# Kernel tuning notes

Hardware: AMD Instinct MI355X
Metric: run time of the kernel (lower is better)

## Reference

```python
import jax, jax.numpy as jnp
import numpy as np

V, SMAX, D, H, L, DFF, W = 32000, 1024, 1024, 16, 2, 4096, 256
HD = D // H
EPS = 1e-6


def setup_inputs() -> dict:
    key = jax.random.key(0)
    ks = jax.random.split(key, 20)
    s = lambda k, shape, scale=0.02: jax.random.normal(k, shape, dtype=jnp.float32) * scale
    return {
        "input_ids": jax.random.randint(ks[0], (2, SMAX), 0, V, dtype=jnp.int64),
        "emb": s(ks[1], (V, D)),
        "pos": s(ks[2], (SMAX, D)),
        "norm1_w": jnp.ones((L, D), jnp.float32),
        "norm2_w": jnp.ones((L, D), jnp.float32),
        "wq": s(ks[3], (L, D, D)), "bq": jnp.zeros((L, D), jnp.float32),
        "wk": s(ks[4], (L, D, D)), "bk": jnp.zeros((L, D), jnp.float32),
        "wv": s(ks[5], (L, D, D)), "bv": jnp.zeros((L, D), jnp.float32),
        "wo": s(ks[6], (L, D, D)), "bo": jnp.zeros((L, D), jnp.float32),
        "w1": s(ks[7], (L, D, DFF)), "b1": jnp.zeros((L, DFF), jnp.float32),
        "w2": s(ks[8], (L, DFF, D)), "b2": jnp.zeros((L, D), jnp.float32),
        "normf_w": jnp.ones((D,), jnp.float32),
    }


def rms(x, w):
    return x * jax.lax.rsqrt(jnp.mean(x * x, axis=-1, keepdims=True) + EPS) * w


def reference(input_ids, emb, pos, norm1_w, norm2_w, wq, bq, wk, bk, wv, bv,
              wo, bo, w1, b1, w2, b2, normf_w):
    B, S = input_ids.shape
    x = emb[input_ids] + pos[:S]  # [B,S,D]
    # sliding-window causal mask: attend to j with 0 <= i-j < W
    i = jnp.arange(S)[:, None]
    j = jnp.arange(S)[None, :]
    mask = (j <= i) & (i - j < W)  # [S,S]
    neg = jnp.asarray(-1e9, x.dtype)
    for l in range(L):
        h = rms(x, norm1_w[l])
        q = (h @ wq[l] + bq[l]).reshape(B, S, H, HD)
        k = (h @ wk[l] + bk[l]).reshape(B, S, H, HD)
        v = (h @ wv[l] + bv[l]).reshape(B, S, H, HD)
        scores = jnp.einsum('bqhd,bkhd->bhqk', q, k) / np.sqrt(HD).astype(np.float32)
        scores = jnp.where(mask[None, None], scores, neg)
        attn = jax.nn.softmax(scores, axis=-1)
        o = jnp.einsum('bhqk,bkhd->bqhd', attn, v).reshape(B, S, D)
        x = x + (o @ wo[l] + bo[l])
        h2 = rms(x, norm2_w[l])
        x = x + (jax.nn.gelu(h2 @ w1[l] + b1[l], approximate=False) @ w2[l] + b2[l])
    x = rms(x, normf_w)
    logits = x @ emb.T  # tied lm_head
    return logits
```

## Files before the change

kernel.cpp:

```cpp
#include <hip/hip_runtime.h>
#include <hip/hip_bf16.h>
#include <cstdint>

typedef __bf16 bf16;
typedef __bf16 bf16x8 __attribute__((ext_vector_type(8)));
typedef __bf16 bf16x4 __attribute__((ext_vector_type(4)));
typedef float  f32x4  __attribute__((ext_vector_type(4)));

constexpr int V_    = 32000;
constexpr int SMAX_ = 1024;
constexpr int D_    = 1024;
constexpr int H_    = 16;
constexpr int L_    = 2;
constexpr int DFF_  = 4096;
constexpr int WIN_  = 256;
constexpr int B_    = 2;
constexpr int M_    = B_ * SMAX_;

#define SBAR0_() __builtin_amdgcn_sched_barrier(0)
#define HWBAR_() { __builtin_amdgcn_s_barrier(); SBAR0_(); }
#define LGKM0_() { asm volatile("s_waitcnt lgkmcnt(0)" ::: "memory"); SBAR0_(); }

__global__ __launch_bounds__(512) void gemm_lm_bdirect(
    const bf16* __restrict__ A, const bf16* __restrict__ BT,
    float* __restrict__ outf, int Nn)
{
  constexpr int KK = 1024, NT = 16;
  __shared__ __align__(16) bf16 ldsA[2][16384];

  const int t = threadIdx.x, lane = t & 63, w = t >> 6;
  const int l16 = lane & 15, lh = lane >> 4;
  const int wm = w >> 2, wn = w & 3;

  const int nloc = gridDim.x >> 3;
  const int wg = (blockIdx.x & 7) * nloc + (blockIdx.x >> 3);
  const long m0 = (long)(wg & 7) * 256;
  const long n0 = (long)(wg >> 3) * 256;

  auto STGA = [&](int c, int k0) {
    #pragma unroll
    for (int q = 0; q < 4; ++q) {
      int row = q * 64 + (t >> 3);
      int sl  = (t & 7) ^ (row & 7);
      const bf16* g = A + (m0 + row) * (long)KK + k0 + sl * 8;
      __builtin_amdgcn_global_load_lds(
          (const __attribute__((address_space(1))) uint32_t*)g,
          (__attribute__((address_space(3))) uint32_t*)(&ldsA[c][q * 4096 + t * 8]),
          16, 0, 0);
    }
  };
  auto LDA = [&](int c, int mi, int ks) -> bf16x8 {
    int row = wm * 128 + mi * 16 + l16;
    int sl  = (ks * 4 + lh) ^ (row & 7);
    return *(const bf16x8*)(&ldsA[c][row * 64 + sl * 8]);
  };
  auto BADDR = [&](int ni, int kk) -> const bf16* {
    return BT + (n0 + wn * 64 + ni * 16 + l16) * (long)KK + kk + lh * 8;
  };

  f32x4 acc[8][4] = {};
  bf16x8 a[8], b0[4], b1[4];

  STGA(0, 0);
  SBAR0_();
  #pragma unroll
  for (int ni = 0; ni < 4; ++ni) b0[ni] = *(const bf16x8*)BADDR(ni, 0);

  for (int j = 0; j < NT; ++j) {
    const int c = j & 1;
    const int kc = j * 64;
    const int kn = (kc + 64) & (KK - 1);
    asm volatile("s_waitcnt vmcnt(4)" ::: "memory"); SBAR0_();
    HWBAR_();
    #pragma unroll
    for (int mi = 0; mi < 8; ++mi) a[mi] = LDA(c, mi, 0);
    #pragma unroll
    for (int ni = 0; ni < 4; ++ni) b1[ni] = *(const bf16x8*)BADDR(ni, kc + 32);
    LGKM0_();
    asm volatile("s_waitcnt vmcnt(4)" ::: "memory"); SBAR0_();
    __builtin_amdgcn_s_setprio(1);
    #pragma unroll
    for (int mi = 0; mi < 8; ++mi)
      #pragma unroll
      for (int ni = 0; ni < 4; ++ni)
        acc[mi][ni] = __builtin_amdgcn_mfma_f32_16x16x32_bf16(a[mi], b0[ni], acc[mi][ni], 0, 0, 0);
    __builtin_amdgcn_s_setprio(0);
    SBAR0_();
    #pragma unroll
    for (int mi = 0; mi < 8; ++mi) a[mi] = LDA(c, mi, 1);
    STGA(c ^ 1, kn);
    SBAR0_();
    #pragma unroll
    for (int ni = 0; ni < 4; ++ni) b0[ni] = *(const bf16x8*)BADDR(ni, kn);
    LGKM0_();
    asm volatile("s_waitcnt vmcnt(8)" ::: "memory"); SBAR0_();
    __builtin_amdgcn_s_setprio(1);
    #pragma unroll
    for (int mi = 0; mi < 8; ++mi)
      #pragma unroll
      for (int ni = 0; ni < 4; ++ni)
        acc[mi][ni] = __builtin_amdgcn_mfma_f32_16x16x32_bf16(a[mi], b1[ni], acc[mi][ni], 0, 0, 0);
    __builtin_amdgcn_s_setprio(0);
  }

  asm volatile("s_waitcnt vmcnt(0) lgkmcnt(0)" ::: "memory");
  #pragma unroll
  for (int mi = 0; mi < 8; ++mi)
    #pragma unroll
    for (int ni = 0; ni < 4; ++ni)
      #pragma unroll
      for (int rr = 0; rr < 4; ++rr) {
        long row = m0 + wm * 128 + mi * 16 + lh * 4 + rr;
        long col = n0 + wn * 64 + ni * 16 + l16;
        outf[row * Nn + col] = acc[mi][ni][rr];
      }
}

template<int BM, int EPI>
__global__ __launch_bounds__(256, (BM == 128 ? 2 : 3)) void gemm_deep(
    const bf16* __restrict__ A, const bf16* __restrict__ BT,
    const float* __restrict__ bias, float* __restrict__ resid,
    bf16* __restrict__ outb, float* __restrict__ outf,
    int Nn, int Kk, int nbyMask, int nbyShift)
{
  constexpr int WR = BM / 32;
  constexpr int CA = BM / 64;
  constexpr int LPS = CA + 2;
  __shared__ __align__(16) bf16 ldsA[4 * BM * 32];
  __shared__ __align__(16) bf16 ldsB[4 * 4096];

  const int t = threadIdx.x, lane = t & 63, w = t >> 6;
  const int l16 = lane & 15, lh = lane >> 4;
  const int wm = w >> 1, wn = w & 1;

  const int nwg = gridDim.x, bid = blockIdx.x;
  const int nloc = nwg >> 3;
  const int wg = (bid & 7) * nloc + (bid >> 3);
  const long m0 = (long)(wg & nbyMask) * BM;
  const long n0 = (long)(wg >> nbyShift) * 128;

  auto STGA = [&](bf16* dst, int k0) {
    #pragma unroll
    for (int j = 0; j < CA; ++j) {
      int p = j * 4096 + t * 16;
      int row = p >> 6;
      int sl = ((p >> 4) & 3) ^ (row & 3);
      const bf16* g = A + (m0 + row) * (long)Kk + k0 + sl * 8;
      __builtin_amdgcn_global_load_lds(
          (const __attribute__((address_space(1))) uint32_t*)g,
          (__attribute__((address_space(3))) uint32_t*)(dst + j * 2048 + w * 512),
          16, 0, 0);
    }
  };
  auto STGB = [&](bf16* dst, int k0) {
    #pragma unroll
    for (int j = 0; j < 2; ++j) {
      int p = j * 4096 + t * 16;
      int row = p >> 6;
      int sl = ((p >> 4) & 3) ^ (row & 3);
      const bf16* g = BT + (n0 + row) * (long)Kk + k0 + sl * 8;
      __builtin_amdgcn_global_load_lds(
          (const __attribute__((address_space(1))) uint32_t*)g,
          (__attribute__((address_space(3))) uint32_t*)(dst + j * 2048 + w * 512),
          16, 0, 0);
    }
  };
  auto LDF = [&](const bf16* base, int rowb) -> bf16x8 {
    int row = rowb + l16;
    return *(const bf16x8*)(base + row * 32 + ((lh ^ (l16 & 3)) << 3));
  };

  f32x4 acc[WR][4] = {};

  STGA(ldsA,               0);  STGB(ldsB,        0);
  STGA(ldsA + BM * 32,    32);  STGB(ldsB + 4096, 32);
  STGA(ldsA + 2 * BM * 32, 64); STGB(ldsB + 8192, 64);
  int kNext = 96;

  const int NT = Kk >> 5;
  for (int i = 0; i < NT; ++i) {
    const int cur = i & 3, nb = (i + 3) & 3;
    if constexpr (LPS == 4) { asm volatile("s_waitcnt vmcnt(8)" ::: "memory"); }
    else                    { asm volatile("s_waitcnt vmcnt(6)" ::: "memory"); }
    SBAR0_();
    HWBAR_();
    const bf16* Ac = ldsA + cur * BM * 32;
    const bf16* Bc = ldsB + cur * 4096;
    bf16x8 af[WR], bb[4];
    #pragma unroll
    for (int mi = 0; mi < WR; ++mi) af[mi] = LDF(Ac, wm * (WR * 16) + mi * 16);
    #pragma unroll
    for (int ni = 0; ni < 4; ++ni) bb[ni] = LDF(Bc, wn * 64 + ni * 16);
    STGA(ldsA + nb * BM * 32, kNext);
    STGB(ldsB + nb * 4096, kNext);
    kNext += 32; if (kNext == Kk) kNext = 0;
    LGKM0_();
    __builtin_amdgcn_s_setprio(1);
    #pragma unroll
    for (int mi = 0; mi < WR; ++mi)
      #pragma unroll
      for (int ni = 0; ni < 4; ++ni)
        acc[mi][ni] = __builtin_amdgcn_mfma_f32_16x16x32_bf16(af[mi], bb[ni], acc[mi][ni], 0, 0, 0);
    __builtin_amdgcn_s_setprio(0);
  }

  #pragma unroll
  for (int mi = 0; mi < WR; ++mi)
    #pragma unroll
    for (int ni = 0; ni < 4; ++ni)
      #pragma unroll
      for (int rr = 0; rr < 4; ++rr) {
        long row = m0 + wm * (WR * 16) + mi * 16 + lh * 4 + rr;
        long col = n0 + wn * 64 + ni * 16 + l16;
        float v = acc[mi][ni][rr];
        if (EPI == 0) {
          outb[row * Nn + col] = (bf16)(v + bias[col]);
        } else if (EPI == 1) {
          float xx = v + bias[col];
          outb[row * Nn + col] = (bf16)(0.5f * xx * (1.0f + erff(xx * 0.70710678118654752f)));
        } else if (EPI == 2) {
          resid[row * Nn + col] += v + bias[col];
        } else {
          outf[row * Nn + col] = v;
        }
      }
}

__global__ __launch_bounds__(256) void attn_swa(
    const bf16* __restrict__ qkv, bf16* __restrict__ o)
{
  constexpr int PADK = 72;
  constexpr int PADV = 40;
  __shared__ bf16 Qs[64 * PADK];
  __shared__ bf16 Ks[32 * PADK];
  __shared__ bf16 Vt[64 * PADV];
  __shared__ bf16 Ps[4][16 * PADV];

  const int bid = blockIdx.x;
  const int qb = bid & 15;
  const int h  = (bid >> 4) & 15;
  const int b  = bid >> 8;
  const int q0 = qb * 64;
  const int t = threadIdx.x, lane = t & 63, w = t >> 6;
  const int l16 = lane & 15, lh = lane >> 4;

  #pragma unroll
  for (int i = 0; i < 2; i++) {
    int e = t + i * 256;
    int row = e >> 3, cc = e & 7;
    uint4 g = *(const uint4*)(qkv + ((long)(b * SMAX_ + q0 + row)) * 3072 + h * 64 + cc * 8);
    *(uint4*)(Qs + row * PADK + cc * 8) = g;
  }
  __syncthreads();
  bf16x8 aq[2];
  const int qrow = w * 16 + l16;
  #pragma unroll
  for (int ks = 0; ks < 2; ks++)
    aq[ks] = *(const bf16x8*)(Qs + qrow * PADK + ks * 32 + lh * 8);

  float m_run[4], l_run[4];
  f32x4 oacc[4];
  #pragma unroll
  for (int rr = 0; rr < 4; rr++) { m_run[rr] = -1e30f; l_run[rr] = 0.0f; }
  #pragma unroll
  for (int n = 0; n < 4; n++) oacc[n] = (f32x4){0.f, 0.f, 0.f, 0.f};

  const int tlo = q0 - (WIN_ - 1);
  const int jlo = (tlo <= 0) ? 0 : (tlo & ~31);
  const int iq  = q0 + w * 16 + lh * 4;

  for (int j0 = jlo; j0 < q0 + 64; j0 += 32) {
    __syncthreads();
    {
      int row = t >> 3, cc = t & 7;
      long base = ((long)(b * SMAX_ + j0 + row)) * 3072 + h * 64 + cc * 8;
      uint4 gk = *(const uint4*)(qkv + base + 1024);
      *(uint4*)(Ks + row * PADK + cc * 8) = gk;
      bf16x8 vv = *(const bf16x8*)(qkv + base + 2048);
      #pragma unroll
      for (int j = 0; j < 8; j++)
        Vt[(cc * 8 + j) * PADV + row] = vv[j];
    }
    __syncthreads();

    f32x4 s[2] = {(f32x4){0.f,0.f,0.f,0.f}, (f32x4){0.f,0.f,0.f,0.f}};
    #pragma unroll
    for (int nt = 0; nt < 2; nt++)
      #pragma unroll
      for (int ks = 0; ks < 2; ks++) {
        bf16x8 bk = *(const bf16x8*)(Ks + (nt * 16 + l16) * PADK + ks * 32 + lh * 8);
        s[nt] = __builtin_amdgcn_mfma_f32_16x16x32_bf16(aq[ks], bk, s[nt], 0, 0, 0);
      }

    float sc[2][4];
    #pragma unroll
    for (int nt = 0; nt < 2; nt++)
      #pragma unroll
      for (int rr = 0; rr < 4; rr++) {
        int i = iq + rr;
        int j = j0 + nt * 16 + l16;
        float v = s[nt][rr] * 0.125f;
        bool ok = (j <= i) && (i - j < WIN_);
        sc[nt][rr] = ok ? v : -1e30f;
      }

    float pb[2][4], alpha[4];
    #pragma unroll
    for (int rr = 0; rr < 4; rr++) {
      float mt = fmaxf(sc[0][rr], sc[1][rr]);
      #pragma unroll
      for (int off = 1; off < 16; off <<= 1) mt = fmaxf(mt, __shfl_xor(mt, off, 64));
      float mn = fmaxf(m_run[rr], mt);
      float a = __expf(m_run[rr] - mn);
      m_run[rr] = mn; alpha[rr] = a;
      float p0 = __expf(sc[0][rr] - mn);
      float p1 = __expf(sc[1][rr] - mn);
      pb[0][rr] = p0; pb[1][rr] = p1;
      float ls = p0 + p1;
      #pragma unroll
      for (int off = 1; off < 16; off <<= 1) ls += __shfl_xor(ls, off, 64);
      l_run[rr] = l_run[rr] * a + ls;
    }
    #pragma unroll
    for (int n = 0; n < 4; n++)
      #pragma unroll
      for (int rr = 0; rr < 4; rr++) oacc[n][rr] *= alpha[rr];

    #pragma unroll
    for (int rr = 0; rr < 4; rr++) {
      int prow = lh * 4 + rr;
      Ps[w][prow * PADV + l16]      = (bf16)pb[0][rr];
      Ps[w][prow * PADV + 16 + l16] = (bf16)pb[1][rr];
    }
    __syncthreads();

    bf16x8 pa = *(const bf16x8*)(&Ps[w][l16 * PADV + lh * 8]);
    #pragma unroll
    for (int n = 0; n < 4; n++) {
      bf16x8 bv = *(const bf16x8*)(Vt + (n * 16 + l16) * PADV + lh * 8);
      oacc[n] = __builtin_amdgcn_mfma_f32_16x16x32_bf16(pa, bv, oacc[n], 0, 0, 0);
    }
  }

  #pragma unroll
  for (int rr = 0; rr < 4; rr++) {
    int i = iq + rr;
    float inv = 1.0f / l_run[rr];
    #pragma unroll
    for (int n = 0; n < 4; n++)
      o[((long)(b * SMAX_ + i)) * D_ + h * 64 + n * 16 + l16] = (bf16)(oacc[n][rr] * inv);
  }
}

__global__ __launch_bounds__(256) void transpose_cvt(
    const float* __restrict__ src, bf16* __restrict__ dst,
    int Kk, int Nn, long srcL, long dstL)
{
  __shared__ float tile[32][33];
  const int tx = threadIdx.x, ty = threadIdx.y;
  const long n0 = (long)blockIdx.x * 32, k0 = (long)blockIdx.y * 32;
  src += (long)blockIdx.z * srcL;
  dst += (long)blockIdx.z * dstL;
  #pragma unroll
  for (int i = 0; i < 4; i++)
    tile[ty + i * 8][tx] = src[(k0 + ty + i * 8) * Nn + n0 + tx];
  __syncthreads();
  #pragma unroll
  for (int i = 0; i < 4; i++)
    dst[(n0 + ty + i * 8) * Kk + k0 + tx] = (bf16)tile[tx][ty + i * 8];
}

__global__ __launch_bounds__(256) void cvt_bf16(
    const float* __restrict__ src, bf16* __restrict__ dst, long n4)
{
  long i = (long)blockIdx.x * 256 + threadIdx.x;
  if (i >= n4) return;
  float4 v = ((const float4*)src)[i];
  bf16x4 o; o[0] = (bf16)v.x; o[1] = (bf16)v.y; o[2] = (bf16)v.z; o[3] = (bf16)v.w;
  ((bf16x4*)dst)[i] = o;
}

__global__ __launch_bounds__(256) void pack_bqkv(
    const float* __restrict__ bq, const float* __restrict__ bk,
    const float* __restrict__ bv, float* __restrict__ out)
{
  int i = blockIdx.x * 256 + threadIdx.x;
  if (i >= L_ * 3072) return;
  int l = i / 3072, c = i % 3072;
  float v = (c < 1024) ? bq[l * 1024 + c]
          : (c < 2048) ? bk[l * 1024 + c - 1024]
                       : bv[l * 1024 + c - 2048];
  out[i] = v;
}

__global__ __launch_bounds__(256) void embed_k(
    const int* __restrict__ ids, const float* __restrict__ emb,
    const float* __restrict__ pos, float* __restrict__ x)
{
  const int m = blockIdx.x, t = threadIdx.x;
  const int id = ids[m];
  const int s = m & (SMAX_ - 1);
  float4 e = ((const float4*)(emb + (long)id * D_))[t];
  float4 p = ((const float4*)(pos + (long)s * D_))[t];
  float4 rr; rr.x = e.x + p.x; rr.y = e.y + p.y; rr.z = e.z + p.z; rr.w = e.w + p.w;
  ((float4*)(x + (long)m * D_))[t] = rr;
}

__global__ __launch_bounds__(256) void rmsnorm_k(
    const float* __restrict__ x, const float* __restrict__ wgt,
    bf16* __restrict__ out)
{
  __shared__ float red[4];
  const int m = blockIdx.x, t = threadIdx.x;
  float4 v = ((const float4*)(x + (long)m * D_))[t];
  float ss = v.x * v.x + v.y * v.y + v.z * v.z + v.w * v.w;
  #pragma unroll
  for (int off = 1; off < 64; off <<= 1) ss += __shfl_xor(ss, off, 64);
  const int lane = t & 63, w = t >> 6;
  if (lane == 0) red[w] = ss;
  __syncthreads();
  float tot = red[0] + red[1] + red[2] + red[3];
  float rs = rsqrtf(tot * (1.0f / D_) + 1e-6f);
  float4 g = ((const float4*)wgt)[t];
  bf16x4 o;
  o[0] = (bf16)(v.x * rs * g.x); o[1] = (bf16)(v.y * rs * g.y);
  o[2] = (bf16)(v.z * rs * g.z); o[3] = (bf16)(v.w * rs * g.w);
  ((bf16x4*)(out + (long)m * D_))[t] = o;
}

extern "C" void kernel_launch(void* const* d_in, const int* in_sizes, int n_in,
                              void* d_out, int out_size, void* d_ws, size_t ws_size,
                              hipStream_t stream)
{
  const int*   ids = (const int*)d_in[0];
  const float* emb = (const float*)d_in[1];
  const float* pos = (const float*)d_in[2];
  const float* n1w = (const float*)d_in[3];
  const float* n2w = (const float*)d_in[4];
  const float* wq  = (const float*)d_in[5];
  const float* bq  = (const float*)d_in[6];
  const float* wk  = (const float*)d_in[7];
  const float* bk  = (const float*)d_in[8];
  const float* wv  = (const float*)d_in[9];
  const float* bv  = (const float*)d_in[10];
  const float* wo  = (const float*)d_in[11];
  const float* bo  = (const float*)d_in[12];
  const float* w1  = (const float*)d_in[13];
  const float* b1  = (const float*)d_in[14];
  const float* w2  = (const float*)d_in[15];
  const float* b2  = (const float*)d_in[16];
  const float* nfw = (const float*)d_in[17];

  char* p = (char*)d_ws;
  auto alloc = [&](size_t bytes) {
    char* rr = p; p += (bytes + 255) & ~(size_t)255; return rr;
  };
  bf16*  wqkv_t = (bf16*) alloc((size_t)L_ * 3 * 1024 * 1024 * 2);
  bf16*  wo_t   = (bf16*) alloc((size_t)L_ * 1024 * 1024 * 2);
  bf16*  w1_t   = (bf16*) alloc((size_t)L_ * 4096 * 1024 * 2);
  bf16*  w2_t   = (bf16*) alloc((size_t)L_ * 1024 * 4096 * 2);
  bf16*  emb_bf = (bf16*) alloc((size_t)V_ * D_ * 2);
  float* bqkv   = (float*)alloc((size_t)L_ * 3072 * 4);
  float* x      = (float*)alloc((size_t)M_ * D_ * 4);
  bf16*  hbuf   = (bf16*) alloc((size_t)M_ * D_ * 2);
  bf16*  qkv    = (bf16*) alloc((size_t)M_ * 3072 * 2);
  bf16*  obuf   = (bf16*) alloc((size_t)M_ * D_ * 2);
  bf16*  ff     = (bf16*) alloc((size_t)M_ * DFF_ * 2);

  const dim3 b32(32, 8, 1);
  transpose_cvt<<<dim3(32, 32, L_),  b32, 0, stream>>>(wq, wqkv_t,                1024, 1024, 1024 * 1024, 3 * 1024 * 1024);
  transpose_cvt<<<dim3(32, 32, L_),  b32, 0, stream>>>(wk, wqkv_t + 1024 * 1024,  1024, 1024, 1024 * 1024, 3 * 1024 * 1024);
  transpose_cvt<<<dim3(32, 32, L_),  b32, 0, stream>>>(wv, wqkv_t + 2*1024*1024,  1024, 1024, 1024 * 1024, 3 * 1024 * 1024);
  transpose_cvt<<<dim3(32, 32, L_),  b32, 0, stream>>>(wo, wo_t,                  1024, 1024, 1024 * 1024, 1024 * 1024);
  transpose_cvt<<<dim3(128, 32, L_), b32, 0, stream>>>(w1, w1_t,                  1024, 4096, 1024 * 4096, 4096 * 1024);
  transpose_cvt<<<dim3(32, 128, L_), b32, 0, stream>>>(w2, w2_t,                  4096, 1024, 4096 * 1024, 1024 * 4096);
  cvt_bf16<<<32000, 256, 0, stream>>>(emb, emb_bf, (long)V_ * D_ / 4);
  pack_bqkv<<<24, 256, 0, stream>>>(bq, bk, bv, bqkv);
  embed_k<<<M_, 256, 0, stream>>>(ids, emb, pos, x);

  for (int l = 0; l < L_; l++) {
    rmsnorm_k<<<M_, 256, 0, stream>>>(x, n1w + l * D_, hbuf);
    gemm_deep<128, 0><<<dim3(16 * 24), 256, 0, stream>>>(
        hbuf, wqkv_t + (size_t)l * 3 * 1024 * 1024, bqkv + l * 3072,
        nullptr, qkv, nullptr, 3072, 1024, 15, 4);
    attn_swa<<<B_ * H_ * (SMAX_ / 64), 256, 0, stream>>>(qkv, obuf);
    gemm_deep<64, 2><<<dim3(32 * 8), 256, 0, stream>>>(
        obuf, wo_t + (size_t)l * 1024 * 1024, bo + l * D_,
        x, nullptr, nullptr, 1024, 1024, 31, 5);
    rmsnorm_k<<<M_, 256, 0, stream>>>(x, n2w + l * D_, hbuf);
    gemm_deep<128, 1><<<dim3(16 * 32), 256, 0, stream>>>(
        hbuf, w1_t + (size_t)l * 4096 * 1024, b1 + l * DFF_,
        nullptr, ff, nullptr, 4096, 1024, 15, 4);
    gemm_deep<64, 2><<<dim3(32 * 8), 256, 0, stream>>>(
        ff, w2_t + (size_t)l * 1024 * 4096, b2 + l * D_,
        x, nullptr, nullptr, 1024, 4096, 31, 5);
  }
  rmsnorm_k<<<M_, 256, 0, stream>>>(x, nfw, hbuf);
  gemm_lm_bdirect<<<dim3(8 * (V_ / 256)), 512, 0, stream>>>(
      hbuf, emb_bf, (float*)d_out, V_);
}
```

Measured before the change: 650.1 us.

## Restructure LM-head and layer GEMMs with LDS-staged B tiles and new pipelines

Measured after the change: 640.9 us. About the same (-1.4%).

```diff
diff --git a/kernel.cpp b/kernel.cpp
--- a/kernel.cpp
+++ b/kernel.cpp
@@ -21,21 +21,22 @@
 #define HWBAR_() { __builtin_amdgcn_s_barrier(); SBAR0_(); }
 #define LGKM0_() { asm volatile("s_waitcnt lgkmcnt(0)" ::: "memory"); SBAR0_(); }
 
-__global__ __launch_bounds__(512) void gemm_lm_bdirect(
+__global__ __launch_bounds__(512, 1) void gemm_lm2(
     const bf16* __restrict__ A, const bf16* __restrict__ BT,
     float* __restrict__ outf, int Nn)
 {
   constexpr int KK = 1024, NT = 16;
-  __shared__ __align__(16) bf16 ldsA[2][16384];
+  __shared__ __align__(16) bf16 ldsA[3][16384];
+  __shared__ __align__(16) bf16 ldsB[3][8192];
 
   const int t = threadIdx.x, lane = t & 63, w = t >> 6;
   const int l16 = lane & 15, lh = lane >> 4;
-  const int wm = w >> 2, wn = w & 3;
+  const int wm = w >> 1, wn = w & 1;
 
   const int nloc = gridDim.x >> 3;
   const int wg = (blockIdx.x & 7) * nloc + (blockIdx.x >> 3);
   const long m0 = (long)(wg & 7) * 256;
-  const long n0 = (long)(wg >> 3) * 256;
+  const long n0 = (long)(wg >> 3) * 128;
 
   auto STGA = [&](int c, int k0) {
     #pragma unroll
@@ -49,85 +50,95 @@
           16, 0, 0);
     }
   };
+  auto STGB = [&](int c, int k0) {
+    #pragma unroll
+    for (int q = 0; q < 2; ++q) {
+      int row = q * 64 + (t >> 3);
+      int sl  = (t & 7) ^ (row & 7);
+      const bf16* g = BT + (n0 + row) * (long)KK + k0 + sl * 8;
+      __builtin_amdgcn_global_load_lds(
+          (const __attribute__((address_space(1))) uint32_t*)g,
+          (__attribute__((address_space(3))) uint32_t*)(&ldsB[c][q * 4096 + t * 8]),
+          16, 0, 0);
+    }
+  };
   auto LDA = [&](int c, int mi, int ks) -> bf16x8 {
-    int row = wm * 128 + mi * 16 + l16;
+    int row = wm * 64 + mi * 16 + l16;
     int sl  = (ks * 4 + lh) ^ (row & 7);
     return *(const bf16x8*)(&ldsA[c][row * 64 + sl * 8]);
   };
-  auto BADDR = [&](int ni, int kk) -> const bf16* {
-    return BT + (n0 + wn * 64 + ni * 16 + l16) * (long)KK + kk + lh * 8;
-  };
-
-  f32x4 acc[8][4] = {};
-  bf16x8 a[8], b0[4], b1[4];
-
-  STGA(0, 0);
-  SBAR0_();
-  #pragma unroll
-  for (int ni = 0; ni < 4; ++ni) b0[ni] = *(const bf16x8*)BADDR(ni, 0);
+  auto LDB = [&](int c, int ni, int ks) -> bf16x8 {
+    int row = wn * 64 + ni * 16 + l16;
+    int sl  = (ks * 4 + lh) ^ (row & 7);
+    return *(const bf16x8*)(&ldsB[c][row * 64 + sl * 8]);
+  };
+
+  f32x4 acc[4][4] = {};
+  bf16x8 a[4], b[4];
+
+  STGA(0, 0);  STGB(0, 0);
+  STGA(1, 64); STGB(1, 64);
+  int kNext = 128, stg = 2, c = 0;
 
   for (int j = 0; j < NT; ++j) {
-    const int c = j & 1;
-    const int kc = j * 64;
-    const int kn = (kc + 64) & (KK - 1);
-    asm volatile("s_waitcnt vmcnt(4)" ::: "memory"); SBAR0_();
+    asm volatile("s_waitcnt vmcnt(6)" ::: "memory"); SBAR0_();
     HWBAR_();
     #pragma unroll
-    for (int mi = 0; mi < 8; ++mi) a[mi] = LDA(c, mi, 0);
-    #pragma unroll
-    for (int ni = 0; ni < 4; ++ni) b1[ni] = *(const bf16x8*)BADDR(ni, kc + 32);
+    for (int mi = 0; mi < 4; ++mi) a[mi] = LDA(c, mi, 0);
+    #pragma unroll
+    for (int ni = 0; ni < 4; ++ni) b[ni] = LDB(c, ni, 0);
+    STGA(stg, kNext);
     LGKM0_();
-    asm volatile("s_waitcnt vmcnt(4)" ::: "memory"); SBAR0_();
     __builtin_amdgcn_s_setprio(1);
     #pragma unroll
-    for (int mi = 0; mi < 8; ++mi)
+    for (int mi = 0; mi < 4; ++mi)
       #pragma unroll
       for (int ni = 0; ni < 4; ++ni)
-        acc[mi][ni] = __builtin_amdgcn_mfma_f32_16x16x32_bf16(a[mi], b0[ni], acc[mi][ni], 0, 0, 0);
+        acc[mi][ni] = __builtin_amdgcn_mfma_f32_16x16x32_bf16(a[mi], b[ni], acc[mi][ni], 0, 0, 0);
     __builtin_amdgcn_s_setprio(0);
-    SBAR0_();
-    #pragma unroll
-    for (int mi = 0; mi < 8; ++mi) a[mi] = LDA(c, mi, 1);
-    STGA(c ^ 1, kn);
-    SBAR0_();
-    #pragma unroll
-    for (int ni = 0; ni < 4; ++ni) b0[ni] = *(const bf16x8*)BADDR(ni, kn);
+    HWBAR_();
+    #pragma unroll
+    for (int mi = 0; mi < 4; ++mi) a[mi] = LDA(c, mi, 1);
+    #pragma unroll
+    for (int ni = 0; ni < 4; ++ni) b[ni] = LDB(c, ni, 1);
+    STGB(stg, kNext);
     LGKM0_();
-    asm volatile("s_waitcnt vmcnt(8)" ::: "memory"); SBAR0_();
     __builtin_amdgcn_s_setprio(1);
     #pragma unroll
-    for (int mi = 0; mi < 8; ++mi)
+    for (int mi = 0; mi < 4; ++mi)
       #pragma unroll
       for (int ni = 0; ni < 4; ++ni)
-        acc[mi][ni] = __builtin_amdgcn_mfma_f32_16x16x32_bf16(a[mi], b1[ni], acc[mi][ni], 0, 0, 0);
+        acc[mi][ni] = __builtin_amdgcn_mfma_f32_16x16x32_bf16(a[mi], b[ni], acc[mi][ni], 0, 0, 0);
     __builtin_amdgcn_s_setprio(0);
+    kNext += 64; if (kNext == KK) kNext = 0;
+    stg += 1; if (stg == 3) stg = 0;
+    c   += 1; if (c   == 3) c   = 0;
   }
 
   asm volatile("s_waitcnt vmcnt(0) lgkmcnt(0)" ::: "memory");
   #pragma unroll
-  for (int mi = 0; mi < 8; ++mi)
+  for (int mi = 0; mi < 4; ++mi)
     #pragma unroll
     for (int ni = 0; ni < 4; ++ni)
       #pragma unroll
       for (int rr = 0; rr < 4; ++rr) {
-        long row = m0 + wm * 128 + mi * 16 + lh * 4 + rr;
+        long row = m0 + wm * 64 + mi * 16 + lh * 4 + rr;
         long col = n0 + wn * 64 + ni * 16 + l16;
         outf[row * Nn + col] = acc[mi][ni][rr];
       }
 }
 
 template<int BM, int EPI>
-__global__ __launch_bounds__(256, (BM == 128 ? 2 : 3)) void gemm_deep(
+__global__ __launch_bounds__(256) void gemm_l2(
     const bf16* __restrict__ A, const bf16* __restrict__ BT,
     const float* __restrict__ bias, float* __restrict__ resid,
     bf16* __restrict__ outb, float* __restrict__ outf,
     int Nn, int Kk, int nbyMask, int nbyShift)
 {
-  constexpr int WR = BM / 32;
-  constexpr int CA = BM / 64;
-  constexpr int LPS = CA + 2;
-  __shared__ __align__(16) bf16 ldsA[4 * BM * 32];
-  __shared__ __align__(16) bf16 ldsB[4 * 4096];
+  constexpr int MR = BM / 32;
+  constexpr int CA = BM / 32;
+  __shared__ __align__(16) bf16 ldsA[2][BM * 64];
+  __shared__ __align__(16) bf16 ldsB[2][8192];
 
   const int t = threadIdx.x, lane = t & 63, w = t >> 6;
   const int l16 = lane & 15, lh = lane >> 4;
@@ -139,78 +150,88 @@
   const long m0 = (long)(wg & nbyMask) * BM;
   const long n0 = (long)(wg >> nbyShift) * 128;
 
-  auto STGA = [&](bf16* dst, int k0) {
-    #pragma unroll
-    for (int j = 0; j < CA; ++j) {
-      int p = j * 4096 + t * 16;
-      int row = p >> 6;
-      int sl = ((p >> 4) & 3) ^ (row & 3);
+  auto STGA = [&](int c, int k0) {
+    #pragma unroll
+    for (int q = 0; q < CA; ++q) {
+      int row = q * 32 + (t >> 3);
+      int sl  = (t & 7) ^ (row & 7);
       const bf16* g = A + (m0 + row) * (long)Kk + k0 + sl * 8;
       __builtin_amdgcn_global_load_lds(
           (const __attribute__((address_space(1))) uint32_t*)g,
-          (__attribute__((address_space(3))) uint32_t*)(dst + j * 2048 + w * 512),
+          (__attribute__((address_space(3))) uint32_t*)(&ldsA[c][q * 2048 + t * 8]),
           16, 0, 0);
     }
   };
-  auto STGB = [&](bf16* dst, int k0) {
-    #pragma unroll
-    for (int j = 0; j < 2; ++j) {
-      int p = j * 4096 + t * 16;
-      int row = p >> 6;
-      int sl = ((p >> 4) & 3) ^ (row & 3);
+  auto STGB = [&](int c, int k0) {
+    #pragma unroll
+    for (int q = 0; q < 4; ++q) {
+      int row = q * 32 + (t >> 3);
+      int sl  = (t & 7) ^ (row & 7);
       const bf16* g = BT + (n0 + row) * (long)Kk + k0 + sl * 8;
       __builtin_amdgcn_global_load_lds(
           (const __attribute__((address_space(1))) uint32_t*)g,
-          (__attribute__((address_space(3))) uint32_t*)(dst + j * 2048 + w * 512),
+          (__attribute__((address_space(3))) uint32_t*)(&ldsB[c][q * 2048 + t * 8]),
           16, 0, 0);
     }
   };
-  auto LDF = [&](const bf16* base, int rowb) -> bf16x8 {
-    int row = rowb + l16;
-    return *(const bf16x8*)(base + row * 32 + ((lh ^ (l16 & 3)) << 3));
-  };
-
-  f32x4 acc[WR][4] = {};
-
-  STGA(ldsA,               0);  STGB(ldsB,        0);
-  STGA(ldsA + BM * 32,    32);  STGB(ldsB + 4096, 32);
-  STGA(ldsA + 2 * BM * 32, 64); STGB(ldsB + 8192, 64);
-  int kNext = 96;
-
-  const int NT = Kk >> 5;
-  for (int i = 0; i < NT; ++i) {
-    const int cur = i & 3, nb = (i + 3) & 3;
-    if constexpr (LPS == 4) { asm volatile("s_waitcnt vmcnt(8)" ::: "memory"); }
-    else                    { asm volatile("s_waitcnt vmcnt(6)" ::: "memory"); }
-    SBAR0_();
+  auto LDA = [&](int c, int mi, int ks) -> bf16x8 {
+    int row = wm * (BM / 2) + mi * 16 + l16;
+    int sl  = (ks * 4 + lh) ^ (row & 7);
+    return *(const bf16x8*)(&ldsA[c][row * 64 + sl * 8]);
+  };
+  auto LDB = [&](int c, int ni, int ks) -> bf16x8 {
+    int row = wn * 64 + ni * 16 + l16;
+    int sl  = (ks * 4 + lh) ^ (row & 7);
+    return *(const bf16x8*)(&ldsB[c][row * 64 + sl * 8]);
+  };
+
+  f32x4 acc[MR][4] = {};
+  bf16x8 a[MR], b[4];
+
+  STGA(0, 0); STGB(0, 0);
+  int kNext = 64;
+
+  const int NT = Kk >> 6;
+  for (int j = 0; j < NT; ++j) {
+    const int c = j & 1;
+    asm volatile("s_waitcnt vmcnt(0)" ::: "memory"); SBAR0_();
     HWBAR_();
-    const bf16* Ac = ldsA + cur * BM * 32;
-    const bf16* Bc = ldsB + cur * 4096;
-    bf16x8 af[WR], bb[4];
-    #pragma unroll
-    for (int mi = 0; mi < WR; ++mi) af[mi] = LDF(Ac, wm * (WR * 16) + mi * 16);
-    #pragma unroll
-    for (int ni = 0; ni < 4; ++ni) bb[ni] = LDF(Bc, wn * 64 + ni * 16);
-    STGA(ldsA + nb * BM * 32, kNext);
-    STGB(ldsB + nb * 4096, kNext);
-    kNext += 32; if (kNext == Kk) kNext = 0;
+    #pragma unroll
+    for (int mi = 0; mi < MR; ++mi) a[mi] = LDA(c, mi, 0);
+    #pragma unroll
+    for (int ni = 0; ni < 4; ++ni) b[ni] = LDB(c, ni, 0);
+    STGA(c ^ 1, kNext); STGB(c ^ 1, kNext);
     LGKM0_();
     __builtin_amdgcn_s_setprio(1);
     #pragma unroll
-    for (int mi = 0; mi < WR; ++mi)
+    for (int mi = 0; mi < MR; ++mi)
       #pragma unroll
       for (int ni = 0; ni < 4; ++ni)
-        acc[mi][ni] = __builtin_amdgcn_mfma_f32_16x16x32_bf16(af[mi], bb[ni], acc[mi][ni], 0, 0, 0);
+        acc[mi][ni] = __builtin_amdgcn_mfma_f32_16x16x32_bf16(a[mi], b[ni], acc[mi][ni], 0, 0, 0);
     __builtin_amdgcn_s_setprio(0);
+    HWBAR_();
+    #pragma unroll
+    for (int mi = 0; mi < MR; ++mi) a[mi] = LDA(c, mi, 1);
+    #pragma unroll
+    for (int ni = 0; ni < 4; ++ni) b[ni] = LDB(c, ni, 1);
+    LGKM0_();
+    __builtin_amdgcn_s_setprio(1);
+    #pragma unroll
+    for (int mi = 0; mi < MR; ++mi)
+      #pragma unroll
+      for (int ni = 0; ni < 4; ++ni)
+        acc[mi][ni] = __builtin_amdgcn_mfma_f32_16x16x32_bf16(a[mi], b[ni], acc[mi][ni], 0, 0, 0);
+    __builtin_amdgcn_s_setprio(0);
+    kNext += 64; if (kNext == Kk) kNext = 0;
   }
 
   #pragma unroll
-  for (int mi = 0; mi < WR; ++mi)
+  for (int mi = 0; mi < MR; ++mi)
     #pragma unroll
     for (int ni = 0; ni < 4; ++ni)
       #pragma unroll
       for (int rr = 0; rr < 4; ++rr) {
-        long row = m0 + wm * (WR * 16) + mi * 16 + lh * 4 + rr;
+        long row = m0 + wm * (BM / 2) + mi * 16 + lh * 4 + rr;
         long col = n0 + wn * 64 + ni * 16 + l16;
         float v = acc[mi][ni][rr];
         if (EPI == 0) {
@@ -480,22 +501,22 @@
 
   for (int l = 0; l < L_; l++) {
     rmsnorm_k<<<M_, 256, 0, stream>>>(x, n1w + l * D_, hbuf);
-    gemm_deep<128, 0><<<dim3(16 * 24), 256, 0, stream>>>(
+    gemm_l2<128, 0><<<dim3(16 * 24), 256, 0, stream>>>(
         hbuf, wqkv_t + (size_t)l * 3 * 1024 * 1024, bqkv + l * 3072,
         nullptr, qkv, nullptr, 3072, 1024, 15, 4);
     attn_swa<<<B_ * H_ * (SMAX_ / 64), 256, 0, stream>>>(qkv, obuf);
-    gemm_deep<64, 2><<<dim3(32 * 8), 256, 0, stream>>>(
+    gemm_l2<64, 2><<<dim3(32 * 8), 256, 0, stream>>>(
         obuf, wo_t + (size_t)l * 1024 * 1024, bo + l * D_,
         x, nullptr, nullptr, 1024, 1024, 31, 5);
     rmsnorm_k<<<M_, 256, 0, stream>>>(x, n2w + l * D_, hbuf);
-    gemm_deep<128, 1><<<dim3(16 * 32), 256, 0, stream>>>(
+    gemm_l2<128, 1><<<dim3(16 * 32), 256, 0, stream>>>(
         hbuf, w1_t + (size_t)l * 4096 * 1024, b1 + l * DFF_,
         nullptr, ff, nullptr, 4096, 1024, 15, 4);
-    gemm_deep<64, 2><<<dim3(32 * 8), 256, 0, stream>>>(
+    gemm_l2<64, 2><<<dim3(32 * 8), 256, 0, stream>>>(
         ff, w2_t + (size_t)l * 1024 * 4096, b2 + l * D_,
         x, nullptr, nullptr, 1024, 4096, 31, 5);
   }
   rmsnorm_k<<<M_, 256, 0, stream>>>(x, nfw, hbuf);
-  gemm_lm_bdirect<<<dim3(8 * (V_ / 256)), 512, 0, stream>>>(
+  gemm_lm2<<<dim3(8 * (V_ / 128)), 512, 0, stream>>>(
       hbuf, emb_bf, (float*)d_out, V_);
 }
```
